# Kernel optimization log

Hardware: AMD Instinct MI355X
Metric: run time of the kernel (lower is better)

The kernel has to match this reference:

```python
import jax, jax.numpy as jnp
import numpy as np
from jax import lax

BS, T, NN, F_IN = 4, 32, 128, 64
HID, HEADS, NC, LD, RH = 64, 4, 32, 64, 256
E = 2048
NEG_SLOPE = 0.2


def setup_inputs() -> dict:
    key = jax.random.key(0)
    ks = jax.random.split(key, 20)
    f32 = jnp.float32
    def n(k, shape, s=0.05):
        return jax.random.normal(k, shape, f32) * s
    G4 = 4 * RH
    return {
        "x": jax.random.normal(ks[0], (BS, T, NN, F_IN), f32),
        "edge_index": jax.random.randint(ks[1], (2, E), 0, NN),
        "W1": n(ks[2], (F_IN, HEADS * HID)),
        "as1": n(ks[3], (HEADS, HID)), "ad1": n(ks[4], (HEADS, HID)),
        "b1": jnp.zeros((HEADS * HID,), f32),
        "W2": n(ks[5], (HEADS * HID, HEADS * HID)),
        "as2": n(ks[6], (HEADS, HID)), "ad2": n(ks[7], (HEADS, HID)),
        "b2": jnp.zeros((HEADS * HID,), f32),
        "W3": n(ks[8], (HEADS * HID, HID)),
        "as3": n(ks[9], (1, HID)), "ad3": n(ks[10], (1, HID)),
        "b3": jnp.zeros((HID,), f32),
        "Wih_f": n(ks[11], (G4, HID)), "Whh_f": n(ks[12], (G4, RH)),
        "bih_f": jnp.zeros((G4,), f32), "bhh_f": jnp.zeros((G4,), f32),
        "Wih_b": n(ks[13], (G4, HID)), "Whh_b": n(ks[14], (G4, RH)),
        "bih_b": jnp.zeros((G4,), f32), "bhh_b": jnp.zeros((G4,), f32),
        "Wmu": n(ks[15], (NC * LD, 2 * RH)), "bmu": jnp.zeros((NC * LD,), f32),
        "Wlv": n(ks[16], (NC * LD, 2 * RH)), "blv": jnp.zeros((NC * LD,), f32),
        "Wpi": n(ks[17], (NC, 2 * RH)), "bpi": jnp.zeros((NC,), f32),
    }


def _lstm_dir(seq, Wih, Whh, bih, bhh, rh):
    # seq: [T, B, D]; torch gate order i, f, g, o
    B = seq.shape[1]
    h0 = jnp.zeros((B, rh), seq.dtype)
    c0 = jnp.zeros((B, rh), seq.dtype)
    def step(carry, xt):
        h, c = carry
        g = xt @ Wih.T + h @ Whh.T + bih + bhh
        i, f, gg, o = jnp.split(g, 4, axis=-1)
        c = jax.nn.sigmoid(f) * c + jax.nn.sigmoid(i) * jnp.tanh(gg)
        h = jax.nn.sigmoid(o) * jnp.tanh(c)
        return (h, c), None
    (hT, _), _ = lax.scan(step, (h0, c0), seq)
    return hT


def reference(x, edge_index, W1, as1, ad1, b1, W2, as2, ad2, b2,
              W3, as3, ad3, b3,
              Wih_f, Whh_f, bih_f, bhh_f, Wih_b, Whh_b, bih_b, bhh_b,
              Wmu, bmu, Wlv, blv, Wpi, bpi):
    bs, T_, nn_, fin = x.shape
    G = bs * T_
    N = G * nn_
    xt = x.reshape(N, fin)
    # batch the per-graph edge list with node offsets, then add self loops (PyG default)
    off = jnp.arange(G, dtype=edge_index.dtype) * nn_
    src = (edge_index[0][None, :] + off[:, None]).reshape(-1)
    dst = (edge_index[1][None, :] + off[:, None]).reshape(-1)
    loop = jnp.arange(N, dtype=edge_index.dtype)
    src = jnp.concatenate([src, loop])
    dst = jnp.concatenate([dst, loop])

    def gat(h_in, W, a_s, a_d, b, heads):
        C = W.shape[1] // heads
        h = (h_in @ W).reshape(N, heads, C)
        a_src = jnp.sum(h * a_s, axis=-1)  # [N, H]
        a_dst = jnp.sum(h * a_d, axis=-1)
        e = jax.nn.leaky_relu(a_src[src] + a_dst[dst], NEG_SLOPE)  # [Etot, H]
        m = jax.ops.segment_max(e, dst, num_segments=N)
        m = jnp.where(jnp.isfinite(m), m, 0.0)
        ex = jnp.exp(e - m[dst])
        den = jax.ops.segment_sum(ex, dst, num_segments=N)
        alpha = ex / (den[dst] + 1e-16)
        out = jax.ops.segment_sum(alpha[:, :, None] * h[src], dst, num_segments=N)
        return out.reshape(N, heads * C) + b

    h = jax.nn.relu(gat(xt, W1, as1, ad1, b1, HEADS))
    h = jax.nn.relu(gat(h, W2, as2, ad2, b2, HEADS))
    h = jax.nn.relu(gat(h, W3, as3, ad3, b3, 1))

    batch_idx = jnp.repeat(jnp.arange(G), nn_)
    graph_embs = jax.ops.segment_sum(h, batch_idx, num_segments=G).reshape(bs, T_, -1)
    seq = jnp.transpose(graph_embs, (1, 0, 2))  # [T, B, D]
    h_f = _lstm_dir(seq, Wih_f, Whh_f, bih_f, bhh_f, RH)
    h_b = _lstm_dir(seq[::-1], Wih_b, Whh_b, bih_b, bhh_b, RH)
    feat = jnp.concatenate([h_f, h_b], axis=-1)  # [B, 2*RH]
    mu = (feat @ Wmu.T + bmu).reshape(bs, NC, LD)
    logvar = (feat @ Wlv.T + blv).reshape(bs, NC, LD)
    pi_logits = feat @ Wpi.T + bpi
    return (mu, logvar, pi_logits)
```

## Files before the change

kernel.cpp:

```cpp
#include <hip/hip_runtime.h>
#include <hip/hip_bf16.h>
#include <cstdint>

#define NLOC 128
#define NGRAPH 128
#define NNODE 16384
#define EBASE 2048

typedef _Float16 half2v __attribute__((ext_vector_type(2)));
typedef _Float16 f16x8 __attribute__((ext_vector_type(8)));
typedef float f32x4 __attribute__((ext_vector_type(4)));

__device__ __forceinline__ float sigf(float x) { return 1.f / (1.f + __expf(-x)); }
__device__ __forceinline__ float tanhfast(float x) {
    float e = __expf(2.f * x);
    return 1.f - 2.f / (e + 1.f);
}
__device__ __forceinline__ uint32_t packh2(float a, float b) {
    half2v v;
    v.x = (_Float16)a; v.y = (_Float16)b;
    return __builtin_bit_cast(uint32_t, v);
}
__device__ __forceinline__ float dot2(uint32_t w, uint32_t h, float acc) {
#if __has_builtin(__builtin_amdgcn_fdot2)
    return __builtin_amdgcn_fdot2(__builtin_bit_cast(half2v, w),
                                  __builtin_bit_cast(half2v, h), acc, false);
#else
    half2v wv = __builtin_bit_cast(half2v, w);
    half2v hv = __builtin_bit_cast(half2v, h);
    return acc + (float)wv.x * (float)hv.x + (float)wv.y * (float)hv.y;
#endif
}

__global__ __launch_bounds__(256) void prep_kernel(const int* __restrict__ ei,
                                                   float* __restrict__ Adj,
                                                   const float* __restrict__ W1,
                                                   const float* __restrict__ W2,
                                                   const float* __restrict__ W3,
                                                   _Float16* __restrict__ W1t,
                                                   _Float16* __restrict__ W2t,
                                                   _Float16* __restrict__ W3t,
                                                   const float* __restrict__ Whh_f,
                                                   const float* __restrict__ Whh_b,
                                                   uint32_t* __restrict__ wreg,
                                                   uint32_t* __restrict__ wtail) {
    int b = blockIdx.x, tid = threadIdx.x;
    if (b < 128) {
        __shared__ int rowA[NLOC];
        int v = b;
        if (tid < NLOC) rowA[tid] = 0;
        __syncthreads();
        const int* srcs = ei;
        const int* dsts = ei + EBASE;
        int e0 = tid * 8;
#pragma unroll
        for (int k = 0; k < 8; ++k)
            if (dsts[e0 + k] == v) atomicAdd(&rowA[srcs[e0 + k]], 1);
        __syncthreads();
        if (tid < NLOC) Adj[v * NLOC + tid] = (float)rowA[tid] + (tid == v ? 1.f : 0.f);
    } else if (b < 144) {
        int i = (b - 128) * 1024 + tid * 4;
        int n = i >> 6, k = i & 63;
#pragma unroll
        for (int j = 0; j < 4; ++j) W1t[n * 64 + k + j] = (_Float16)W1[(size_t)(k + j) * 256 + n];
    } else if (b < 208) {
        int i = (b - 144) * 1024 + tid * 4;
        int n = i >> 8, k = i & 255;
#pragma unroll
        for (int j = 0; j < 4; ++j) W2t[n * 256 + k + j] = (_Float16)W2[(size_t)(k + j) * 256 + n];
    } else if (b < 224) {
        int i = (b - 208) * 1024 + tid * 4;
        int n = i >> 8, k = i & 255;
#pragma unroll
        for (int j = 0; j < 4; ++j) W3t[n * 256 + k + j] = (_Float16)W3[(size_t)(k + j) * 64 + n];
    } else {
        int gid = (b - 224) * 256 + tid;
        int dir = gid >> 10, row = gid & 1023;
        const float* src = (dir ? Whh_b : Whh_f) + (size_t)row * 256;
        uint4* wr4 = (uint4*)wreg;
#pragma unroll
        for (int i = 0; i < 24; ++i) {
            uint4 v;
            v.x = packh2(src[i * 8 + 0], src[i * 8 + 1]);
            v.y = packh2(src[i * 8 + 2], src[i * 8 + 3]);
            v.z = packh2(src[i * 8 + 4], src[i * 8 + 5]);
            v.w = packh2(src[i * 8 + 6], src[i * 8 + 7]);
            wr4[(size_t)(dir * 24 + i) * 1024 + row] = v;
        }
        uint4* wt4 = (uint4*)wtail;
#pragma unroll
        for (int ku = 0; ku < 8; ++ku) {
            const float* s8 = src + 192 + ku * 8;
            uint4 v;
            v.x = packh2(s8[0], s8[1]);
            v.y = packh2(s8[2], s8[3]);
            v.z = packh2(s8[4], s8[5]);
            v.w = packh2(s8[6], s8[7]);
            wt4[(size_t)(dir * 8 + ku) * 1024 + row] = v;
        }
    }
}

template <int K, int NL, int NF, bool POOLX>
__global__ __launch_bounds__(512) void fl_kernel(const float* __restrict__ A,
                                                 const _Float16* __restrict__ Wg,
                                                 const float* __restrict__ a_s,
                                                 const float* __restrict__ a_d,
                                                 const float* __restrict__ Adj,
                                                 const float* __restrict__ bias,
                                                 const float* __restrict__ Wih_f, const float* __restrict__ bif, const float* __restrict__ bhf,
                                                 const float* __restrict__ Wih_b, const float* __restrict__ bib, const float* __restrict__ bhb,
                                                 float* __restrict__ outG) {
    constexpr int HL = NL / 64;
    constexpr int NT = NL / 64;
    constexpr int WPH = 4 / HL;
    constexpr int LDA = K + 4;
    constexpr int LDB = 68;
    constexpr int LDH = 136;
    constexpr int ASB = 128 * LDA * 2;
    constexpr int HTB = NL * LDH * 2;
    constexpr int R1 = (ASB > HTB) ? ASB : HTB;
    constexpr int R2 = 128 * LDH * 2;
    __shared__ __align__(16) char raw[R1 + R2];
    _Float16* As = (_Float16*)raw;
    _Float16* Ht = (_Float16*)raw;
    _Float16* Bs = (_Float16*)(raw + R1);
    _Float16* Wt = (_Float16*)(raw + R1);
    __shared__ float as_l[128 * HL];
    __shared__ float ad_l[128 * HL];
    __shared__ float den_l[128];
    __shared__ float as_part[4][128];
    __shared__ float ad_part[4][128];
    __shared__ float psum[8][64];
    __shared__ float emb[64];

    int g = blockIdx.x, tid = threadIdx.x;
    int foff = blockIdx.y * NL;
    int lane = tid & 63, w = tid >> 6;
    int wm = w >> 2, wn = w & 3;
    int col = lane & 15, kg = lane >> 4;
    size_t base = (size_t)g * 128;

    float asc[NT], adc[NT];
#pragma unroll
    for (int nt = 0; nt < NT; ++nt) {
        int f = foff + (wn * NT + nt) * 16 + col;
        asc[nt] = a_s[f];
        adc[nt] = a_d[f];
    }
    {
        const float* src = A + base * K;
        for (int i = tid; i < 128 * K / 2; i += 512) {
            int m = (2 * i) / K, k = (2 * i) % K;
            float2 v = *(const float2*)(src + (size_t)m * K + k);
            *(uint32_t*)&As[m * LDA + k] = packh2(v.x, v.y);
        }
    }
    f32x4 acc[4][NT];
#pragma unroll
    for (int mt = 0; mt < 4; ++mt)
#pragma unroll
        for (int nt = 0; nt < NT; ++nt) acc[mt][nt] = (f32x4){0.f, 0.f, 0.f, 0.f};
#pragma unroll 1
    for (int kc = 0; kc < K / 64; ++kc) {
        __syncthreads();
        for (int j = tid; j < NL * 8; j += 512) {
            int n = j >> 3, ko = (j & 7) * 8;
            *(uint4*)&Bs[n * LDB + ko] = *(const uint4*)&Wg[(size_t)(foff + n) * K + kc * 64 + ko];
        }
        __syncthreads();
        uint4 bf[NT][2];
#pragma unroll
        for (int nt = 0; nt < NT; ++nt) {
            int nb = (wn * NT + nt) * 16 + col;
            bf[nt][0] = *(const uint4*)&Bs[nb * LDB + kg * 8];
            bf[nt][1] = *(const uint4*)&Bs[nb * LDB + 32 + kg * 8];
        }
#pragma unroll
        for (int mt = 0; mt < 4; ++mt) {
            int mrow = wm * 64 + mt * 16 + col;
            uint4 a0 = *(const uint4*)&As[mrow * LDA + kc * 64 + kg * 8];
            uint4 a1 = *(const uint4*)&As[mrow * LDA + kc * 64 + 32 + kg * 8];
#pragma unroll
            for (int nt = 0; nt < NT; ++nt) {
                acc[mt][nt] = __builtin_amdgcn_mfma_f32_16x16x32_f16(
                    __builtin_bit_cast(f16x8, a0), __builtin_bit_cast(f16x8, bf[nt][0]),
                    acc[mt][nt], 0, 0, 0);
                acc[mt][nt] = __builtin_amdgcn_mfma_f32_16x16x32_f16(
                    __builtin_bit_cast(f16x8, a1), __builtin_bit_cast(f16x8, bf[nt][1]),
                    acc[mt][nt], 0, 0, 0);
            }
        }
    }
    __syncthreads();
#pragma unroll
    for (int mt = 0; mt < 4; ++mt) {
        int mb = wm * 64 + mt * 16;
        float pas[4] = {0.f, 0.f, 0.f, 0.f}, pdd[4] = {0.f, 0.f, 0.f, 0.f};
#pragma unroll
        for (int nt = 0; nt < NT; ++nt) {
#pragma unroll
            for (int r = 0; r < 4; ++r) {
                float hv = acc[mt][nt][r];
                pas[r] += hv * asc[nt];
                pdd[r] += hv * adc[nt];
            }
            int f = (wn * NT + nt) * 16 + col;
            *(uint32_t*)&Ht[f * LDH + mb + kg * 4] = packh2(acc[mt][nt][0], acc[mt][nt][1]);
            *(uint32_t*)&Ht[f * LDH + mb + kg * 4 + 2] = packh2(acc[mt][nt][2], acc[mt][nt][3]);
        }
#pragma unroll
        for (int off = 1; off < 16; off <<= 1)
#pragma unroll
            for (int r = 0; r < 4; ++r) {
                pas[r] += __shfl_xor(pas[r], off, 64);
                pdd[r] += __shfl_xor(pdd[r], off, 64);
            }
        if (col == 0) {
#pragma unroll
            for (int r = 0; r < 4; ++r) {
                int m = mb + kg * 4 + r;
                as_part[wn][m] = pas[r];
                ad_part[wn][m] = pdd[r];
            }
        }
    }
    __syncthreads();
    if (tid < 128) {
#pragma unroll
        for (int hl = 0; hl < HL; ++hl) {
            float sa = 0.f, sd = 0.f;
#pragma unroll
            for (int q = 0; q < WPH; ++q) {
                sa += as_part[hl * WPH + q][tid];
                sd += ad_part[hl * WPH + q][tid];
            }
            as_l[tid * HL + hl] = sa;
            ad_l[tid * HL + hl] = sd;
        }
    }
    __syncthreads();
    for (int h = 0; h < HL; ++h) {
        {
            int v = tid >> 2, ub = (tid & 3) * 32;
            float advv = ad_l[v * HL + h];
            const float* arow = Adj + (size_t)v * 128 + ub;
            float dsum = 0.f;
#pragma unroll
            for (int j = 0; j < 16; ++j) {
                float a0 = arow[2 * j], a1 = arow[2 * j + 1];
                float e0 = as_l[(ub + 2 * j) * HL + h] + advv;
                float e1 = as_l[(ub + 2 * j + 1) * HL + h] + advv;
                e0 = (e0 > 0.f) ? e0 : 0.2f * e0;
                e1 = (e1 > 0.f) ? e1 : 0.2f * e1;
                float w0 = a0 * __expf(e0);
                float w1 = a1 * __expf(e1);
                dsum += w0 + w1;
                *(uint32_t*)&Wt[v * LDH + ub + 2 * j] = packh2(w0, w1);
            }
            dsum += __shfl_xor(dsum, 1, 64);
            dsum += __shfl_xor(dsum, 2, 64);
            if ((tid & 3) == 0) den_l[v] = dsum;
        }
        __syncthreads();
        {
            int vt = w;
            f16x8 af[4];
#pragma unroll
            for (int kt = 0; kt < 4; ++kt) {
                uint4 au = *(const uint4*)&Wt[(vt * 16 + col) * LDH + kt * 32 + kg * 8];
                af[kt] = __builtin_bit_cast(f16x8, au);
            }
            float dn[4];
#pragma unroll
            for (int r = 0; r < 4; ++r) dn[r] = den_l[vt * 16 + kg * 4 + r] + 1e-16f;
#pragma unroll
            for (int ft = 0; ft < 4; ++ft) {
                int f = h * 64 + ft * 16 + col;
                f32x4 oacc = {0.f, 0.f, 0.f, 0.f};
#pragma unroll
                for (int kt = 0; kt < 4; ++kt) {
                    uint4 bu = *(const uint4*)&Ht[f * LDH + kt * 32 + kg * 8];
                    oacc = __builtin_amdgcn_mfma_f32_16x16x32_f16(
                        af[kt], __builtin_bit_cast(f16x8, bu), oacc, 0, 0, 0);
                }
                float bv = bias[foff + f];
                if constexpr (!POOLX) {
#pragma unroll
                    for (int r = 0; r < 4; ++r) {
                        int v = vt * 16 + kg * 4 + r;
                        float o = oacc[r] / dn[r] + bv;
                        outG[(size_t)(base + v) * NF + foff + f] = fmaxf(o, 0.f);
                    }
                } else {
                    float ps = 0.f;
#pragma unroll
                    for (int r = 0; r < 4; ++r) ps += fmaxf(oacc[r] / dn[r] + bv, 0.f);
                    ps += __shfl_xor(ps, 16, 64);
                    ps += __shfl_xor(ps, 32, 64);
                    if (kg == 0) psum[w][f] = ps;
                }
            }
        }
        __syncthreads();
    }
    if constexpr (POOLX) {
        if (tid < 64) {
            float s = 0.f;
#pragma unroll
            for (int q = 0; q < 8; ++q) s += psum[q][tid];
            emb[tid] = s;
        }
        __syncthreads();
        int rrow = (g & 31) * 4 + (g >> 5);
        for (int dir = 0; dir < 2; ++dir) {
            const float* W = dir ? Wih_b : Wih_f;
            const float* bi = dir ? bib : bif;
            const float* bh = dir ? bhb : bhf;
            for (int o = tid; o < 1024; o += 512) {
                const float* wr = W + (size_t)o * 64;
                float s = bi[o] + bh[o];
#pragma unroll
                for (int k = 0; k < 64; k += 4) {
                    float4 wv = *(const float4*)(wr + k);
                    s += emb[k] * wv.x + emb[k + 1] * wv.y + emb[k + 2] * wv.z + emb[k + 3] * wv.w;
                }
                outG[dir * 131072 + rrow * 1024 + o] = s;
            }
        }
    }
}

__global__ __launch_bounds__(1024, 1) void lstm_kernel(const float* __restrict__ xp,
                                                       const uint32_t* __restrict__ wreg,
                                                       const uint32_t* __restrict__ wtail,
                                                       float* __restrict__ hT) {
    int blk = blockIdx.x;
    int dir = blk >> 2, batch = blk & 3;
    int t = threadIdx.x;
    uint32_t wa[96];
    {
        const uint4* ra = (const uint4*)wreg + (size_t)dir * 24 * 1024;
#pragma unroll
        for (int i = 0; i < 24; ++i) {
            uint4 v = ra[i * 1024 + t];
            wa[i * 4 + 0] = v.x; wa[i * 4 + 1] = v.y; wa[i * 4 + 2] = v.z; wa[i * 4 + 3] = v.w;
        }
    }
    __shared__ __align__(16) uint4 wlds[8 * 1024];
    __shared__ __align__(16) uint32_t h_pk[128];
    __shared__ float gv[1024];
    {
        const uint4* tsrc = (const uint4*)wtail + (size_t)dir * 8 * 1024;
        for (int i = t; i < 8 * 1024; i += 1024) wlds[i] = tsrc[i];
    }
    if (t < 128) h_pk[t] = 0;
    __syncthreads();
    float creg = 0.f;
    const float* xpb = xp + dir * 131072 + batch * 1024;
#pragma unroll 1
    for (int step = 0; step < 32; ++step) {
        int teff = dir ? (31 - step) : step;
        float xa = xpb[teff * 4096 + t];
        float acc = 0.f;
#pragma unroll
        for (int q = 0; q < 24; ++q) {
            uint4 hq = *(const uint4*)&h_pk[q * 4];
            acc = dot2(wa[q * 4 + 0], hq.x, acc);
            acc = dot2(wa[q * 4 + 1], hq.y, acc);
            acc = dot2(wa[q * 4 + 2], hq.z, acc);
            acc = dot2(wa[q * 4 + 3], hq.w, acc);
        }
#pragma unroll
        for (int ku = 0; ku < 8; ++ku) {
            uint4 hq = *(const uint4*)&h_pk[96 + ku * 4];
            uint4 qa = wlds[ku * 1024 + t];
            acc = dot2(qa.x, hq.x, acc); acc = dot2(qa.y, hq.y, acc);
            acc = dot2(qa.z, hq.z, acc); acc = dot2(qa.w, hq.w, acc);
        }
        gv[t] = acc + xa;
        __syncthreads();
        if (t < 256) {
            float iv = gv[t], fv = gv[t + 256], gg = gv[t + 512], ov = gv[t + 768];
            creg = sigf(fv) * creg + sigf(iv) * tanhfast(gg);
            float hv = sigf(ov) * tanhfast(creg);
            if (step == 31) hT[(size_t)(dir * 4 + batch) * 256 + t] = hv;
            float hnext = __shfl_down(hv, 1, 64);
            if ((t & 1) == 0) h_pk[t >> 1] = packh2(hv, hnext);
        }
        __syncthreads();
    }
}

__global__ __launch_bounds__(256) void heads_kernel(const float* __restrict__ hT,
                                                    const float* __restrict__ Wmu, const float* __restrict__ bmu,
                                                    const float* __restrict__ Wlv, const float* __restrict__ blv,
                                                    const float* __restrict__ Wpi, const float* __restrict__ bpi,
                                                    float* __restrict__ out) {
    __shared__ __align__(16) float feat[4][512];
    int tid = threadIdx.x;
    for (int i = tid; i < 2048; i += 256) {
        int b = i >> 9, j = i & 511;
        int d = j >> 8, jj = j & 255;
        feat[b][j] = hT[(size_t)(d * 4 + b) * 256 + jj];
    }
    __syncthreads();
    int o = blockIdx.x * 32 + (tid >> 3);
    int kp = tid & 7;
    if (o >= 4128) return;
    const float* Wr;
    float bv;
    int kind, m;
    if (o < 2048) { Wr = Wmu + (size_t)o * 512; bv = bmu[o]; kind = 0; m = o; }
    else if (o < 4096) { m = o - 2048; Wr = Wlv + (size_t)m * 512; bv = blv[m]; kind = 1; }
    else { m = o - 4096; Wr = Wpi + (size_t)m * 512; bv = bpi[m]; kind = 2; }
    float s0 = 0.f, s1 = 0.f, s2 = 0.f, s3 = 0.f;
    int k0 = kp * 64;
#pragma unroll
    for (int j = 0; j < 16; ++j) {
        int k = k0 + j * 4;
        float4 wv = *(const float4*)(Wr + k);
        s0 += feat[0][k] * wv.x + feat[0][k + 1] * wv.y + feat[0][k + 2] * wv.z + feat[0][k + 3] * wv.w;
        s1 += feat[1][k] * wv.x + feat[1][k + 1] * wv.y + feat[1][k + 2] * wv.z + feat[1][k + 3] * wv.w;
        s2 += feat[2][k] * wv.x + feat[2][k + 1] * wv.y + feat[2][k + 2] * wv.z + feat[2][k + 3] * wv.w;
        s3 += feat[3][k] * wv.x + feat[3][k + 1] * wv.y + feat[3][k + 2] * wv.z + feat[3][k + 3] * wv.w;
    }
#pragma unroll
    for (int off = 1; off < 8; off <<= 1) {
        s0 += __shfl_xor(s0, off, 64);
        s1 += __shfl_xor(s1, off, 64);
        s2 += __shfl_xor(s2, off, 64);
        s3 += __shfl_xor(s3, off, 64);
    }
    if (kp != 0) return;
    s0 += bv; s1 += bv; s2 += bv; s3 += bv;
    if (kind == 0) {
        out[0 * 2048 + m] = s0; out[1 * 2048 + m] = s1; out[2 * 2048 + m] = s2; out[3 * 2048 + m] = s3;
    } else if (kind == 1) {
        out[8192 + 0 * 2048 + m] = s0; out[8192 + 1 * 2048 + m] = s1;
        out[8192 + 2 * 2048 + m] = s2; out[8192 + 3 * 2048 + m] = s3;
    } else {
        out[16384 + 0 * 32 + m] = s0; out[16384 + 1 * 32 + m] = s1;
        out[16384 + 2 * 32 + m] = s2; out[16384 + 3 * 32 + m] = s3;
    }
}

extern "C" void kernel_launch(void* const* d_in, const int* in_sizes, int n_in,
                              void* d_out, int out_size, void* d_ws, size_t ws_size,
                              hipStream_t stream) {
    const float* x = (const float*)d_in[0];
    const int* ei = (const int*)d_in[1];
    const float* W1 = (const float*)d_in[2];
    const float* as1 = (const float*)d_in[3];
    const float* ad1 = (const float*)d_in[4];
    const float* b1 = (const float*)d_in[5];
    const float* W2 = (const float*)d_in[6];
    const float* as2 = (const float*)d_in[7];
    const float* ad2 = (const float*)d_in[8];
    const float* b2 = (const float*)d_in[9];
    const float* W3 = (const float*)d_in[10];
    const float* as3 = (const float*)d_in[11];
    const float* ad3 = (const float*)d_in[12];
    const float* b3 = (const float*)d_in[13];
    const float* Wih_f = (const float*)d_in[14];
    const float* Whh_f = (const float*)d_in[15];
    const float* bih_f = (const float*)d_in[16];
    const float* bhh_f = (const float*)d_in[17];
    const float* Wih_b = (const float*)d_in[18];
    const float* Whh_b = (const float*)d_in[19];
    const float* bih_b = (const float*)d_in[20];
    const float* bhh_b = (const float*)d_in[21];
    const float* Wmu = (const float*)d_in[22];
    const float* bmu = (const float*)d_in[23];
    const float* Wlv = (const float*)d_in[24];
    const float* blv = (const float*)d_in[25];
    const float* Wpi = (const float*)d_in[26];
    const float* bpi = (const float*)d_in[27];

    float* ws = (float*)d_ws;
    float* buf1 = ws;
    float* buf2 = ws + 4194304;
    float* Adj = ws + 8388608;
    float* xp = ws + 8404992;
    float* hT = ws + 8667136;
    _Float16* W1t = (_Float16*)(ws + 8669184);
    _Float16* W2t = (_Float16*)(ws + 8677376);
    _Float16* W3t = (_Float16*)(ws + 8710144);
    uint32_t* wreg = (uint32_t*)(ws + 8718336);
    uint32_t* wtail = wreg + 196608;
    float* out = (float*)d_out;

    prep_kernel<<<232, 256, 0, stream>>>(ei, Adj, W1, W2, W3, W1t, W2t, W3t,
                                         Whh_f, Whh_b, wreg, wtail);
    fl_kernel<64, 128, 256, false><<<dim3(128, 2), 512, 0, stream>>>(x, W1t, as1, ad1, Adj, b1,
        Wih_f, bih_f, bhh_f, Wih_b, bih_b, bhh_b, buf1);
    fl_kernel<256, 128, 256, false><<<dim3(128, 2), 512, 0, stream>>>(buf1, W2t, as2, ad2, Adj, b2,
        Wih_f, bih_f, bhh_f, Wih_b, bih_b, bhh_b, buf2);
    fl_kernel<256, 64, 64, true><<<dim3(128, 1), 512, 0, stream>>>(buf2, W3t, as3, ad3, Adj, b3,
        Wih_f, bih_f, bhh_f, Wih_b, bih_b, bhh_b, xp);
    lstm_kernel<<<8, 1024, 0, stream>>>(xp, wreg, wtail, hT);
    heads_kernel<<<129, 256, 0, stream>>>(hT, Wmu, bmu, Wlv, blv, Wpi, bpi, out);
}
```

Before: 193.6 us.

## Fuse GAT pipeline and LSTM+heads into two cooperative kernels with grid syncs

Result: slower. 350.3 us (+80.9%).

```diff
diff --git a/kernel.cpp b/kernel.cpp
--- a/kernel.cpp
+++ b/kernel.cpp
@@ -1,6 +1,9 @@
 #include <hip/hip_runtime.h>
 #include <hip/hip_bf16.h>
+#include <hip/hip_cooperative_groups.h>
 #include <cstdint>
+
+namespace cg = cooperative_groups;
 
 #define NLOC 128
 #define NGRAPH 128
@@ -32,85 +35,20 @@
 #endif
 }
 
-__global__ __launch_bounds__(256) void prep_kernel(const int* __restrict__ ei,
-                                                   float* __restrict__ Adj,
-                                                   const float* __restrict__ W1,
-                                                   const float* __restrict__ W2,
-                                                   const float* __restrict__ W3,
-                                                   _Float16* __restrict__ W1t,
-                                                   _Float16* __restrict__ W2t,
-                                                   _Float16* __restrict__ W3t,
-                                                   const float* __restrict__ Whh_f,
-                                                   const float* __restrict__ Whh_b,
-                                                   uint32_t* __restrict__ wreg,
-                                                   uint32_t* __restrict__ wtail) {
-    int b = blockIdx.x, tid = threadIdx.x;
-    if (b < 128) {
-        __shared__ int rowA[NLOC];
-        int v = b;
-        if (tid < NLOC) rowA[tid] = 0;
-        __syncthreads();
-        const int* srcs = ei;
-        const int* dsts = ei + EBASE;
-        int e0 = tid * 8;
-#pragma unroll
-        for (int k = 0; k < 8; ++k)
-            if (dsts[e0 + k] == v) atomicAdd(&rowA[srcs[e0 + k]], 1);
-        __syncthreads();
-        if (tid < NLOC) Adj[v * NLOC + tid] = (float)rowA[tid] + (tid == v ? 1.f : 0.f);
-    } else if (b < 144) {
-        int i = (b - 128) * 1024 + tid * 4;
-        int n = i >> 6, k = i & 63;
-#pragma unroll
-        for (int j = 0; j < 4; ++j) W1t[n * 64 + k + j] = (_Float16)W1[(size_t)(k + j) * 256 + n];
-    } else if (b < 208) {
-        int i = (b - 144) * 1024 + tid * 4;
-        int n = i >> 8, k = i & 255;
-#pragma unroll
-        for (int j = 0; j < 4; ++j) W2t[n * 256 + k + j] = (_Float16)W2[(size_t)(k + j) * 256 + n];
-    } else if (b < 224) {
-        int i = (b - 208) * 1024 + tid * 4;
-        int n = i >> 8, k = i & 255;
-#pragma unroll
-        for (int j = 0; j < 4; ++j) W3t[n * 256 + k + j] = (_Float16)W3[(size_t)(k + j) * 64 + n];
-    } else {
-        int gid = (b - 224) * 256 + tid;
-        int dir = gid >> 10, row = gid & 1023;
-        const float* src = (dir ? Whh_b : Whh_f) + (size_t)row * 256;
-        uint4* wr4 = (uint4*)wreg;
-#pragma unroll
-        for (int i = 0; i < 24; ++i) {
-            uint4 v;
-            v.x = packh2(src[i * 8 + 0], src[i * 8 + 1]);
-            v.y = packh2(src[i * 8 + 2], src[i * 8 + 3]);
-            v.z = packh2(src[i * 8 + 4], src[i * 8 + 5]);
-            v.w = packh2(src[i * 8 + 6], src[i * 8 + 7]);
-            wr4[(size_t)(dir * 24 + i) * 1024 + row] = v;
-        }
-        uint4* wt4 = (uint4*)wtail;
-#pragma unroll
-        for (int ku = 0; ku < 8; ++ku) {
-            const float* s8 = src + 192 + ku * 8;
-            uint4 v;
-            v.x = packh2(s8[0], s8[1]);
-            v.y = packh2(s8[2], s8[3]);
-            v.z = packh2(s8[4], s8[5]);
-            v.w = packh2(s8[6], s8[7]);
-            wt4[(size_t)(dir * 8 + ku) * 1024 + row] = v;
-        }
-    }
-}
-
 template <int K, int NL, int NF, bool POOLX>
-__global__ __launch_bounds__(512) void fl_kernel(const float* __restrict__ A,
-                                                 const _Float16* __restrict__ Wg,
-                                                 const float* __restrict__ a_s,
-                                                 const float* __restrict__ a_d,
-                                                 const float* __restrict__ Adj,
-                                                 const float* __restrict__ bias,
-                                                 const float* __restrict__ Wih_f, const float* __restrict__ bif, const float* __restrict__ bhf,
-                                                 const float* __restrict__ Wih_b, const float* __restrict__ bib, const float* __restrict__ bhb,
-                                                 float* __restrict__ outG) {
+__device__ void fl_body(int g, int foff,
+                        const float* __restrict__ A,
+                        const _Float16* __restrict__ Wg,
+                        const float* __restrict__ a_s,
+                        const float* __restrict__ a_d,
+                        const float* __restrict__ Adj,
+                        const float* __restrict__ bias,
+                        const float* __restrict__ Wih_f, const float* __restrict__ bif, const float* __restrict__ bhf,
+                        const float* __restrict__ Wih_b, const float* __restrict__ bib, const float* __restrict__ bhb,
+                        float* __restrict__ outG,
+                        char* raw, float* as_l, float* ad_l, float* den_l,
+                        float (*as_part)[128], float (*ad_part)[128],
+                        float (*psum)[64], float* emb) {
     constexpr int HL = NL / 64;
     constexpr int NT = NL / 64;
     constexpr int WPH = 4 / HL;
@@ -120,22 +58,12 @@
     constexpr int ASB = 128 * LDA * 2;
     constexpr int HTB = NL * LDH * 2;
     constexpr int R1 = (ASB > HTB) ? ASB : HTB;
-    constexpr int R2 = 128 * LDH * 2;
-    __shared__ __align__(16) char raw[R1 + R2];
     _Float16* As = (_Float16*)raw;
     _Float16* Ht = (_Float16*)raw;
     _Float16* Bs = (_Float16*)(raw + R1);
     _Float16* Wt = (_Float16*)(raw + R1);
-    __shared__ float as_l[128 * HL];
-    __shared__ float ad_l[128 * HL];
-    __shared__ float den_l[128];
-    __shared__ float as_part[4][128];
-    __shared__ float ad_part[4][128];
-    __shared__ float psum[8][64];
-    __shared__ float emb[64];
-
-    int g = blockIdx.x, tid = threadIdx.x;
-    int foff = blockIdx.y * NL;
+
+    int tid = threadIdx.x;
     int lane = tid & 63, w = tid >> 6;
     int wm = w >> 2, wn = w & 3;
     int col = lane & 15, kg = lane >> 4;
@@ -331,33 +259,135 @@
     }
 }
 
-__global__ __launch_bounds__(1024, 1) void lstm_kernel(const float* __restrict__ xp,
-                                                       const uint32_t* __restrict__ wreg,
-                                                       const uint32_t* __restrict__ wtail,
-                                                       float* __restrict__ hT) {
+struct GatArgs {
+    const float* x; const int* ei;
+    const float* W1; const float* as1; const float* ad1; const float* b1;
+    const float* W2; const float* as2; const float* ad2; const float* b2;
+    const float* W3; const float* as3; const float* ad3; const float* b3;
+    const float* Wih_f; const float* bif; const float* bhf;
+    const float* Wih_b; const float* bib; const float* bhb;
+    const float* Whh_f; const float* Whh_b;
+    float* Adj; _Float16* W1t; _Float16* W2t; _Float16* W3t;
+    uint32_t* wreg; uint32_t* wtail;
+    float* buf1; float* buf2; float* xp;
+};
+
+__global__ __launch_bounds__(512) void coop_gat(GatArgs a) {
+    __shared__ __align__(16) char raw[101376];
+    __shared__ float as_l[256], ad_l[256], den_l[128];
+    __shared__ float as_part[4][128], ad_part[4][128];
+    __shared__ float psum[8][64], emb[64];
+    __shared__ int rowA[128];
+    int b = blockIdx.x, tid = threadIdx.x;
+    if (b < 128) {
+        int v = b;
+        if (tid < 128) rowA[tid] = 0;
+        __syncthreads();
+        const int* srcs = a.ei;
+        const int* dsts = a.ei + EBASE;
+        int e0 = tid * 4;
+#pragma unroll
+        for (int k = 0; k < 4; ++k)
+            if (dsts[e0 + k] == v) atomicAdd(&rowA[srcs[e0 + k]], 1);
+        __syncthreads();
+        if (tid < 128) a.Adj[v * NLOC + tid] = (float)rowA[tid] + (tid == v ? 1.f : 0.f);
+    } else if (b < 144) {
+        int i0 = (b - 128) * 1024;
+        for (int i = i0 + tid * 2; i < i0 + 1024; i += 1024) {
+            int n = i >> 6, k = i & 63;
+            a.W1t[n * 64 + k] = (_Float16)a.W1[(size_t)k * 256 + n];
+            a.W1t[n * 64 + k + 1] = (_Float16)a.W1[(size_t)(k + 1) * 256 + n];
+        }
+    } else if (b < 208) {
+        int i0 = (b - 144) * 1024;
+        for (int i = i0 + tid * 2; i < i0 + 1024; i += 1024) {
+            int n = i >> 8, k = i & 255;
+            a.W2t[n * 256 + k] = (_Float16)a.W2[(size_t)k * 256 + n];
+            a.W2t[n * 256 + k + 1] = (_Float16)a.W2[(size_t)(k + 1) * 256 + n];
+        }
+    } else if (b < 224) {
+        int i0 = (b - 208) * 1024;
+        for (int i = i0 + tid * 2; i < i0 + 1024; i += 1024) {
+            int n = i >> 8, k = i & 255;
+            a.W3t[n * 256 + k] = (_Float16)a.W3[(size_t)k * 64 + n];
+            a.W3t[n * 256 + k + 1] = (_Float16)a.W3[(size_t)(k + 1) * 64 + n];
+        }
+    } else if (b < 232) {
+        if (tid < 256) {
+            int gid = (b - 224) * 256 + tid;
+            int dir = gid >> 10, row = gid & 1023;
+            const float* src = (dir ? a.Whh_b : a.Whh_f) + (size_t)row * 256;
+            uint4* wr4 = (uint4*)a.wreg;
+#pragma unroll
+            for (int i = 0; i < 24; ++i) {
+                uint4 v;
+                v.x = packh2(src[i * 8 + 0], src[i * 8 + 1]);
+                v.y = packh2(src[i * 8 + 2], src[i * 8 + 3]);
+                v.z = packh2(src[i * 8 + 4], src[i * 8 + 5]);
+                v.w = packh2(src[i * 8 + 6], src[i * 8 + 7]);
+                wr4[(size_t)(dir * 24 + i) * 1024 + row] = v;
+            }
+            uint4* wt4 = (uint4*)a.wtail;
+#pragma unroll
+            for (int ku = 0; ku < 8; ++ku) {
+                const float* s8 = src + 192 + ku * 8;
+                uint4 v;
+                v.x = packh2(s8[0], s8[1]);
+                v.y = packh2(s8[2], s8[3]);
+                v.z = packh2(s8[4], s8[5]);
+                v.w = packh2(s8[6], s8[7]);
+                wt4[(size_t)(dir * 8 + ku) * 1024 + row] = v;
+            }
+        }
+    }
+    cg::this_grid().sync();
+    int g = b & 127, hb = b >> 7;
+    fl_body<64, 128, 256, false>(g, hb * 128, a.x, a.W1t, a.as1, a.ad1, a.Adj, a.b1,
+        a.Wih_f, a.bif, a.bhf, a.Wih_b, a.bib, a.bhb, a.buf1,
+        raw, as_l, ad_l, den_l, as_part, ad_part, psum, emb);
+    cg::this_grid().sync();
+    fl_body<256, 128, 256, false>(g, hb * 128, a.buf1, a.W2t, a.as2, a.ad2, a.Adj, a.b2,
+        a.Wih_f, a.bif, a.bhf, a.Wih_b, a.bib, a.bhb, a.buf2,
+        raw, as_l, ad_l, den_l, as_part, ad_part, psum, emb);
+    cg::this_grid().sync();
+    if (b < 128)
+        fl_body<256, 64, 64, true>(g, 0, a.buf2, a.W3t, a.as3, a.ad3, a.Adj, a.b3,
+            a.Wih_f, a.bif, a.bhf, a.Wih_b, a.bib, a.bhb, a.xp,
+            raw, as_l, ad_l, den_l, as_part, ad_part, psum, emb);
+}
+
+struct LstmArgs {
+    const float* xp; const uint32_t* wreg; const uint32_t* wtail; float* hT;
+    const float* Wmu; const float* bmu;
+    const float* Wlv; const float* blv;
+    const float* Wpi; const float* bpi;
+    float* out;
+};
+
+__global__ __launch_bounds__(1024, 1) void coop_lstm(LstmArgs a) {
+    __shared__ __align__(16) uint4 wlds[8 * 1024];
+    __shared__ __align__(16) uint32_t h_pk[128];
+    __shared__ float gv[1024];
     int blk = blockIdx.x;
     int dir = blk >> 2, batch = blk & 3;
     int t = threadIdx.x;
     uint32_t wa[96];
     {
-        const uint4* ra = (const uint4*)wreg + (size_t)dir * 24 * 1024;
+        const uint4* ra = (const uint4*)a.wreg + (size_t)dir * 24 * 1024;
 #pragma unroll
         for (int i = 0; i < 24; ++i) {
             uint4 v = ra[i * 1024 + t];
             wa[i * 4 + 0] = v.x; wa[i * 4 + 1] = v.y; wa[i * 4 + 2] = v.z; wa[i * 4 + 3] = v.w;
         }
     }
-    __shared__ __align__(16) uint4 wlds[8 * 1024];
-    __shared__ __align__(16) uint32_t h_pk[128];
-    __shared__ float gv[1024];
     {
-        const uint4* tsrc = (const uint4*)wtail + (size_t)dir * 8 * 1024;
+        const uint4* tsrc = (const uint4*)a.wtail + (size_t)dir * 8 * 1024;
         for (int i = t; i < 8 * 1024; i += 1024) wlds[i] = tsrc[i];
     }
     if (t < 128) h_pk[t] = 0;
     __syncthreads();
     float creg = 0.f;
-    const float* xpb = xp + dir * 131072 + batch * 1024;
+    const float* xpb = a.xp + dir * 131072 + batch * 1024;
 #pragma unroll 1
     for (int step = 0; step < 32; ++step) {
         int teff = dir ? (31 - step) : step;
@@ -384,56 +414,38 @@
             float iv = gv[t], fv = gv[t + 256], gg = gv[t + 512], ov = gv[t + 768];
             creg = sigf(fv) * creg + sigf(iv) * tanhfast(gg);
             float hv = sigf(ov) * tanhfast(creg);
-            if (step == 31) hT[(size_t)(dir * 4 + batch) * 256 + t] = hv;
+            if (step == 31) a.hT[(size_t)(dir * 4 + batch) * 256 + t] = hv;
             float hnext = __shfl_down(hv, 1, 64);
             if ((t & 1) == 0) h_pk[t >> 1] = packh2(hv, hnext);
         }
         __syncthreads();
     }
-}
-
-__global__ __launch_bounds__(256) void heads_kernel(const float* __restrict__ hT,
-                                                    const float* __restrict__ Wmu, const float* __restrict__ bmu,
-                                                    const float* __restrict__ Wlv, const float* __restrict__ blv,
-                                                    const float* __restrict__ Wpi, const float* __restrict__ bpi,
-                                                    float* __restrict__ out) {
-    __shared__ __align__(16) float feat[4][512];
-    int tid = threadIdx.x;
-    for (int i = tid; i < 2048; i += 256) {
-        int b = i >> 9, j = i & 511;
+    __threadfence();
+    cg::this_grid().sync();
+    float* feat = (float*)wlds;
+    for (int i = t; i < 2048; i += 1024) {
+        int bb = i >> 9, j = i & 511;
         int d = j >> 8, jj = j & 255;
-        feat[b][j] = hT[(size_t)(d * 4 + b) * 256 + jj];
+        feat[bb * 512 + j] = a.hT[(size_t)(d * 4 + bb) * 256 + jj];
     }
     __syncthreads();
-    int o = blockIdx.x * 32 + (tid >> 3);
-    int kp = tid & 7;
-    if (o >= 4128) return;
+    int o = blk * 516 + t;
+    if (t >= 516 || o >= 4128) return;
     const float* Wr;
     float bv;
     int kind, m;
-    if (o < 2048) { Wr = Wmu + (size_t)o * 512; bv = bmu[o]; kind = 0; m = o; }
-    else if (o < 4096) { m = o - 2048; Wr = Wlv + (size_t)m * 512; bv = blv[m]; kind = 1; }
-    else { m = o - 4096; Wr = Wpi + (size_t)m * 512; bv = bpi[m]; kind = 2; }
-    float s0 = 0.f, s1 = 0.f, s2 = 0.f, s3 = 0.f;
-    int k0 = kp * 64;
-#pragma unroll
-    for (int j = 0; j < 16; ++j) {
-        int k = k0 + j * 4;
+    if (o < 2048) { Wr = a.Wmu + (size_t)o * 512; bv = a.bmu[o]; kind = 0; m = o; }
+    else if (o < 4096) { m = o - 2048; Wr = a.Wlv + (size_t)m * 512; bv = a.blv[m]; kind = 1; }
+    else { m = o - 4096; Wr = a.Wpi + (size_t)m * 512; bv = a.bpi[m]; kind = 2; }
+    float s0 = bv, s1 = bv, s2 = bv, s3 = bv;
+    for (int k = 0; k < 512; k += 4) {
         float4 wv = *(const float4*)(Wr + k);
-        s0 += feat[0][k] * wv.x + feat[0][k + 1] * wv.y + feat[0][k + 2] * wv.z + feat[0][k + 3] * wv.w;
-        s1 += feat[1][k] * wv.x + feat[1][k + 1] * wv.y + feat[1][k + 2] * wv.z + feat[1][k + 3] * wv.w;
-        s2 += feat[2][k] * wv.x + feat[2][k + 1] * wv.y + feat[2][k + 2] * wv.z + feat[2][k + 3] * wv.w;
-        s3 += feat[3][k] * wv.x + feat[3][k + 1] * wv.y + feat[3][k + 2] * wv.z + feat[3][k + 3] * wv.w;
-    }
-#pragma unroll
-    for (int off = 1; off < 8; off <<= 1) {
-        s0 += __shfl_xor(s0, off, 64);
-        s1 += __shfl_xor(s1, off, 64);
-        s2 += __shfl_xor(s2, off, 64);
-        s3 += __shfl_xor(s3, off, 64);
-    }
-    if (kp != 0) return;
-    s0 += bv; s1 += bv; s2 += bv; s3 += bv;
+        s0 += feat[0 * 512 + k] * wv.x + feat[0 * 512 + k + 1] * wv.y + feat[0 * 512 + k + 2] * wv.z + feat[0 * 512 + k + 3] * wv.w;
+        s1 += feat[1 * 512 + k] * wv.x + feat[1 * 512 + k + 1] * wv.y + feat[1 * 512 + k + 2] * wv.z + feat[1 * 512 + k + 3] * wv.w;
+        s2 += feat[2 * 512 + k] * wv.x + feat[2 * 512 + k + 1] * wv.y + feat[2 * 512 + k + 2] * wv.z + feat[2 * 512 + k + 3] * wv.w;
+        s3 += feat[3 * 512 + k] * wv.x + feat[3 * 512 + k + 1] * wv.y + feat[3 * 512 + k + 2] * wv.z + feat[3 * 512 + k + 3] * wv.w;
+    }
+    float* out = a.out;
     if (kind == 0) {
         out[0 * 2048 + m] = s0; out[1 * 2048 + m] = s1; out[2 * 2048 + m] = s2; out[3 * 2048 + m] = s3;
     } else if (kind == 1) {
@@ -448,56 +460,58 @@
 extern "C" void kernel_launch(void* const* d_in, const int* in_sizes, int n_in,
                               void* d_out, int out_size, void* d_ws, size_t ws_size,
                               hipStream_t stream) {
-    const float* x = (const float*)d_in[0];
-    const int* ei = (const int*)d_in[1];
-    const float* W1 = (const float*)d_in[2];
-    const float* as1 = (const float*)d_in[3];
-    const float* ad1 = (const float*)d_in[4];
-    const float* b1 = (const float*)d_in[5];
-    const float* W2 = (const float*)d_in[6];
-    const float* as2 = (const float*)d_in[7];
-    const float* ad2 = (const float*)d_in[8];
-    const float* b2 = (const float*)d_in[9];
-    const float* W3 = (const float*)d_in[10];
-    const float* as3 = (const float*)d_in[11];
-    const float* ad3 = (const float*)d_in[12];
-    const float* b3 = (const float*)d_in[13];
-    const float* Wih_f = (const float*)d_in[14];
-    const float* Whh_f = (const float*)d_in[15];
-    const float* bih_f = (const float*)d_in[16];
-    const float* bhh_f = (const float*)d_in[17];
-    const float* Wih_b = (const float*)d_in[18];
-    const float* Whh_b = (const float*)d_in[19];
-    const float* bih_b = (const float*)d_in[20];
-    const float* bhh_b = (const float*)d_in[21];
-    const float* Wmu = (const float*)d_in[22];
-    const float* bmu = (const float*)d_in[23];
-    const float* Wlv = (const float*)d_in[24];
-    const float* blv = (const float*)d_in[25];
-    const float* Wpi = (const float*)d_in[26];
-    const float* bpi = (const float*)d_in[27];
-
     float* ws = (float*)d_ws;
-    float* buf1 = ws;
-    float* buf2 = ws + 4194304;
-    float* Adj = ws + 8388608;
-    float* xp = ws + 8404992;
+    GatArgs ga;
+    ga.x = (const float*)d_in[0];
+    ga.ei = (const int*)d_in[1];
+    ga.W1 = (const float*)d_in[2];
+    ga.as1 = (const float*)d_in[3];
+    ga.ad1 = (const float*)d_in[4];
+    ga.b1 = (const float*)d_in[5];
+    ga.W2 = (const float*)d_in[6];
+    ga.as2 = (const float*)d_in[7];
+    ga.ad2 = (const float*)d_in[8];
+    ga.b2 = (const float*)d_in[9];
+    ga.W3 = (const float*)d_in[10];
+    ga.as3 = (const float*)d_in[11];
+    ga.ad3 = (const float*)d_in[12];
+    ga.b3 = (const float*)d_in[13];
+    ga.Wih_f = (const float*)d_in[14];
+    ga.bif = (const float*)d_in[16];
+    ga.bhf = (const float*)d_in[17];
+    ga.Wih_b = (const float*)d_in[18];
+    ga.bib = (const float*)d_in[20];
+    ga.bhb = (const float*)d_in[21];
+    ga.Whh_f = (const float*)d_in[15];
+    ga.Whh_b = (const float*)d_in[19];
+    ga.buf1 = ws;
+    ga.buf2 = ws + 4194304;
+    ga.Adj = ws + 8388608;
+    ga.xp = ws + 8404992;
     float* hT = ws + 8667136;
-    _Float16* W1t = (_Float16*)(ws + 8669184);
-    _Float16* W2t = (_Float16*)(ws + 8677376);
-    _Float16* W3t = (_Float16*)(ws + 8710144);
-    uint32_t* wreg = (uint32_t*)(ws + 8718336);
-    uint32_t* wtail = wreg + 196608;
-    float* out = (float*)d_out;
-
-    prep_kernel<<<232, 256, 0, stream>>>(ei, Adj, W1, W2, W3, W1t, W2t, W3t,
-                                         Whh_f, Whh_b, wreg, wtail);
-    fl_kernel<64, 128, 256, false><<<dim3(128, 2), 512, 0, stream>>>(x, W1t, as1, ad1, Adj, b1,
-        Wih_f, bih_f, bhh_f, Wih_b, bih_b, bhh_b, buf1);
-    fl_kernel<256, 128, 256, false><<<dim3(128, 2), 512, 0, stream>>>(buf1, W2t, as2, ad2, Adj, b2,
-        Wih_f, bih_f, bhh_f, Wih_b, bih_b, bhh_b, buf2);
-    fl_kernel<256, 64, 64, true><<<dim3(128, 1), 512, 0, stream>>>(buf2, W3t, as3, ad3, Adj, b3,
-        Wih_f, bih_f, bhh_f, Wih_b, bih_b, bhh_b, xp);
-    lstm_kernel<<<8, 1024, 0, stream>>>(xp, wreg, wtail, hT);
-    heads_kernel<<<129, 256, 0, stream>>>(hT, Wmu, bmu, Wlv, blv, Wpi, bpi, out);
-}
+    ga.W1t = (_Float16*)(ws + 8669184);
+    ga.W2t = (_Float16*)(ws + 8677376);
+    ga.W3t = (_Float16*)(ws + 8710144);
+    ga.wreg = (uint32_t*)(ws + 8718336);
+    ga.wtail = ga.wreg + 196608;
+
+    LstmArgs la;
+    la.xp = ga.xp;
+    la.wreg = ga.wreg;
+    la.wtail = ga.wtail;
+    la.hT = hT;
+    la.Wmu = (const float*)d_in[22];
+    la.bmu = (const float*)d_in[23];
+    la.Wlv = (const float*)d_in[24];
+    la.blv = (const float*)d_in[25];
+    la.Wpi = (const float*)d_in[26];
+    la.bpi = (const float*)d_in[27];
+    la.out = (float*)d_out;
+
+    void* gargs[] = {&ga};
+    hipLaunchCooperativeKernel((const void*)coop_gat, dim3(256), dim3(512),
+                               gargs, 0, stream);
+    void* largs[] = {&la};
+    hipLaunchCooperativeKernel((const void*)coop_lstm, dim3(8), dim3(1024),
+                               largs, 0, stream);
+}
```

## Fuse output heads into LSTM kernel and read raw fp32 GAT weights directly

Applied to the files above, without the earlier changes.

After: 226.5 us. 16.9% more time.

```diff
diff --git a/kernel.cpp b/kernel.cpp
--- a/kernel.cpp
+++ b/kernel.cpp
@@ -34,16 +34,11 @@
 
 __global__ __launch_bounds__(256) void prep_kernel(const int* __restrict__ ei,
                                                    float* __restrict__ Adj,
-                                                   const float* __restrict__ W1,
-                                                   const float* __restrict__ W2,
-                                                   const float* __restrict__ W3,
-                                                   _Float16* __restrict__ W1t,
-                                                   _Float16* __restrict__ W2t,
-                                                   _Float16* __restrict__ W3t,
                                                    const float* __restrict__ Whh_f,
                                                    const float* __restrict__ Whh_b,
                                                    uint32_t* __restrict__ wreg,
-                                                   uint32_t* __restrict__ wtail) {
+                                                   uint32_t* __restrict__ wtail,
+                                                   int* __restrict__ flag) {
     int b = blockIdx.x, tid = threadIdx.x;
     if (b < 128) {
         __shared__ int rowA[NLOC];
@@ -58,23 +53,9 @@
             if (dsts[e0 + k] == v) atomicAdd(&rowA[srcs[e0 + k]], 1);
         __syncthreads();
         if (tid < NLOC) Adj[v * NLOC + tid] = (float)rowA[tid] + (tid == v ? 1.f : 0.f);
-    } else if (b < 144) {
-        int i = (b - 128) * 1024 + tid * 4;
-        int n = i >> 6, k = i & 63;
-#pragma unroll
-        for (int j = 0; j < 4; ++j) W1t[n * 64 + k + j] = (_Float16)W1[(size_t)(k + j) * 256 + n];
-    } else if (b < 208) {
-        int i = (b - 144) * 1024 + tid * 4;
-        int n = i >> 8, k = i & 255;
-#pragma unroll
-        for (int j = 0; j < 4; ++j) W2t[n * 256 + k + j] = (_Float16)W2[(size_t)(k + j) * 256 + n];
-    } else if (b < 224) {
-        int i = (b - 208) * 1024 + tid * 4;
-        int n = i >> 8, k = i & 255;
-#pragma unroll
-        for (int j = 0; j < 4; ++j) W3t[n * 256 + k + j] = (_Float16)W3[(size_t)(k + j) * 64 + n];
     } else {
-        int gid = (b - 224) * 256 + tid;
+        if (b == 128 && tid == 0) *flag = 0;
+        int gid = (b - 128) * 256 + tid;
         int dir = gid >> 10, row = gid & 1023;
         const float* src = (dir ? Whh_b : Whh_f) + (size_t)row * 256;
         uint4* wr4 = (uint4*)wreg;
@@ -103,7 +84,7 @@
 
 template <int K, int NL, int NF, bool POOLX>
 __global__ __launch_bounds__(512) void fl_kernel(const float* __restrict__ A,
-                                                 const _Float16* __restrict__ Wg,
+                                                 const float* __restrict__ Wg,
                                                  const float* __restrict__ a_s,
                                                  const float* __restrict__ a_d,
                                                  const float* __restrict__ Adj,
@@ -114,6 +95,7 @@
     constexpr int HL = NL / 64;
     constexpr int NT = NL / 64;
     constexpr int WPH = 4 / HL;
+    constexpr int NLSH = (NL == 128) ? 7 : 6;
     constexpr int LDA = K + 4;
     constexpr int LDB = 68;
     constexpr int LDH = 136;
@@ -164,9 +146,12 @@
 #pragma unroll 1
     for (int kc = 0; kc < K / 64; ++kc) {
         __syncthreads();
-        for (int j = tid; j < NL * 8; j += 512) {
-            int n = j >> 3, ko = (j & 7) * 8;
-            *(uint4*)&Bs[n * LDB + ko] = *(const uint4*)&Wg[(size_t)(foff + n) * K + kc * 64 + ko];
+        for (int j = tid; j < NL * 32; j += 512) {
+            int n = j & (NL - 1), kk = j >> NLSH;
+            int k = kc * 64 + 2 * kk;
+            float w0 = Wg[(size_t)k * NF + foff + n];
+            float w1 = Wg[(size_t)(k + 1) * NF + foff + n];
+            *(uint32_t*)&Bs[n * LDB + 2 * kk] = packh2(w0, w1);
         }
         __syncthreads();
         uint4 bf[NT][2];
@@ -334,7 +319,12 @@
 __global__ __launch_bounds__(1024, 1) void lstm_kernel(const float* __restrict__ xp,
                                                        const uint32_t* __restrict__ wreg,
                                                        const uint32_t* __restrict__ wtail,
-                                                       float* __restrict__ hT) {
+                                                       float* __restrict__ hT,
+                                                       const float* __restrict__ Wmu, const float* __restrict__ bmu,
+                                                       const float* __restrict__ Wlv, const float* __restrict__ blv,
+                                                       const float* __restrict__ Wpi, const float* __restrict__ bpi,
+                                                       float* __restrict__ out,
+                                                       int* __restrict__ flag) {
     int blk = blockIdx.x;
     int dir = blk >> 2, batch = blk & 3;
     int t = threadIdx.x;
@@ -390,50 +380,37 @@
         }
         __syncthreads();
     }
-}
-
-__global__ __launch_bounds__(256) void heads_kernel(const float* __restrict__ hT,
-                                                    const float* __restrict__ Wmu, const float* __restrict__ bmu,
-                                                    const float* __restrict__ Wlv, const float* __restrict__ blv,
-                                                    const float* __restrict__ Wpi, const float* __restrict__ bpi,
-                                                    float* __restrict__ out) {
-    __shared__ __align__(16) float feat[4][512];
-    int tid = threadIdx.x;
-    for (int i = tid; i < 2048; i += 256) {
-        int b = i >> 9, j = i & 511;
+    __threadfence();
+    __syncthreads();
+    if (t == 0) {
+        atomicAdd(flag, 1);
+        while (__hip_atomic_load(flag, __ATOMIC_ACQUIRE, __HIP_MEMORY_SCOPE_AGENT) < 8)
+            __builtin_amdgcn_s_sleep(2);
+    }
+    __syncthreads();
+    float* feat = (float*)wlds;
+    for (int i = t; i < 2048; i += 1024) {
+        int bb = i >> 9, j = i & 511;
         int d = j >> 8, jj = j & 255;
-        feat[b][j] = hT[(size_t)(d * 4 + b) * 256 + jj];
-    }
-    __syncthreads();
-    int o = blockIdx.x * 32 + (tid >> 3);
-    int kp = tid & 7;
-    if (o >= 4128) return;
+        feat[bb * 512 + j] = hT[(size_t)(d * 4 + bb) * 256 + jj];
+    }
+    __syncthreads();
+    int o = blk * 516 + t;
+    if (t >= 516 || o >= 4128) return;
     const float* Wr;
     float bv;
     int kind, m;
     if (o < 2048) { Wr = Wmu + (size_t)o * 512; bv = bmu[o]; kind = 0; m = o; }
     else if (o < 4096) { m = o - 2048; Wr = Wlv + (size_t)m * 512; bv = blv[m]; kind = 1; }
     else { m = o - 4096; Wr = Wpi + (size_t)m * 512; bv = bpi[m]; kind = 2; }
-    float s0 = 0.f, s1 = 0.f, s2 = 0.f, s3 = 0.f;
-    int k0 = kp * 64;
-#pragma unroll
-    for (int j = 0; j < 16; ++j) {
-        int k = k0 + j * 4;
+    float s0 = bv, s1 = bv, s2 = bv, s3 = bv;
+    for (int k = 0; k < 512; k += 4) {
         float4 wv = *(const float4*)(Wr + k);
-        s0 += feat[0][k] * wv.x + feat[0][k + 1] * wv.y + feat[0][k + 2] * wv.z + feat[0][k + 3] * wv.w;
-        s1 += feat[1][k] * wv.x + feat[1][k + 1] * wv.y + feat[1][k + 2] * wv.z + feat[1][k + 3] * wv.w;
-        s2 += feat[2][k] * wv.x + feat[2][k + 1] * wv.y + feat[2][k + 2] * wv.z + feat[2][k + 3] * wv.w;
-        s3 += feat[3][k] * wv.x + feat[3][k + 1] * wv.y + feat[3][k + 2] * wv.z + feat[3][k + 3] * wv.w;
-    }
-#pragma unroll
-    for (int off = 1; off < 8; off <<= 1) {
-        s0 += __shfl_xor(s0, off, 64);
-        s1 += __shfl_xor(s1, off, 64);
-        s2 += __shfl_xor(s2, off, 64);
-        s3 += __shfl_xor(s3, off, 64);
-    }
-    if (kp != 0) return;
-    s0 += bv; s1 += bv; s2 += bv; s3 += bv;
+        s0 += feat[0 * 512 + k] * wv.x + feat[0 * 512 + k + 1] * wv.y + feat[0 * 512 + k + 2] * wv.z + feat[0 * 512 + k + 3] * wv.w;
+        s1 += feat[1 * 512 + k] * wv.x + feat[1 * 512 + k + 1] * wv.y + feat[1 * 512 + k + 2] * wv.z + feat[1 * 512 + k + 3] * wv.w;
+        s2 += feat[2 * 512 + k] * wv.x + feat[2 * 512 + k + 1] * wv.y + feat[2 * 512 + k + 2] * wv.z + feat[2 * 512 + k + 3] * wv.w;
+        s3 += feat[3 * 512 + k] * wv.x + feat[3 * 512 + k + 1] * wv.y + feat[3 * 512 + k + 2] * wv.z + feat[3 * 512 + k + 3] * wv.w;
+    }
     if (kind == 0) {
         out[0 * 2048 + m] = s0; out[1 * 2048 + m] = s1; out[2 * 2048 + m] = s2; out[3 * 2048 + m] = s3;
     } else if (kind == 1) {
@@ -483,21 +460,18 @@
     float* Adj = ws + 8388608;
     float* xp = ws + 8404992;
     float* hT = ws + 8667136;
-    _Float16* W1t = (_Float16*)(ws + 8669184);
-    _Float16* W2t = (_Float16*)(ws + 8677376);
-    _Float16* W3t = (_Float16*)(ws + 8710144);
-    uint32_t* wreg = (uint32_t*)(ws + 8718336);
+    uint32_t* wreg = (uint32_t*)(ws + 8669184);
     uint32_t* wtail = wreg + 196608;
+    int* flag = (int*)(wtail + 65536);
     float* out = (float*)d_out;
 
-    prep_kernel<<<232, 256, 0, stream>>>(ei, Adj, W1, W2, W3, W1t, W2t, W3t,
-                                         Whh_f, Whh_b, wreg, wtail);
-    fl_kernel<64, 128, 256, false><<<dim3(128, 2), 512, 0, stream>>>(x, W1t, as1, ad1, Adj, b1,
+    prep_kernel<<<136, 256, 0, stream>>>(ei, Adj, Whh_f, Whh_b, wreg, wtail, flag);
+    fl_kernel<64, 128, 256, false><<<dim3(128, 2), 512, 0, stream>>>(x, W1, as1, ad1, Adj, b1,
         Wih_f, bih_f, bhh_f, Wih_b, bih_b, bhh_b, buf1);
-    fl_kernel<256, 128, 256, false><<<dim3(128, 2), 512, 0, stream>>>(buf1, W2t, as2, ad2, Adj, b2,
+    fl_kernel<256, 128, 256, false><<<dim3(128, 2), 512, 0, stream>>>(buf1, W2, as2, ad2, Adj, b2,
         Wih_f, bih_f, bhh_f, Wih_b, bih_b, bhh_b, buf2);
-    fl_kernel<256, 64, 64, true><<<dim3(128, 1), 512, 0, stream>>>(buf2, W3t, as3, ad3, Adj, b3,
+    fl_kernel<256, 64, 64, true><<<dim3(128, 1), 512, 0, stream>>>(buf2, W3, as3, ad3, Adj, b3,
         Wih_f, bih_f, bhh_f, Wih_b, bih_b, bhh_b, xp);
-    lstm_kernel<<<8, 1024, 0, stream>>>(xp, wreg, wtail, hT);
-    heads_kernel<<<129, 256, 0, stream>>>(hT, Wmu, bmu, Wlv, blv, Wpi, bpi, out);
-}
+    lstm_kernel<<<8, 1024, 0, stream>>>(xp, wreg, wtail, hT,
+                                        Wmu, bmu, Wlv, blv, Wpi, bpi, out, flag);
+}
```
